# Kernel tuning notes

Measured on AMD Instinct MI355X. Metric: run time of the kernel, lower is better.

## Reference

```python
import jax, jax.numpy as jnp
import numpy as np

N = 100000   # nodes
E = 500000   # edges
D = 128      # node_hidden_size
ED = 128     # edge_emb_dim
L = 8        # n_message_passes
H = 4        # num_heads
V = 8192     # node_vocab_size
G = 64       # num_graphs
A = 100      # num_actions
NFLOW = 8
NPOS = 64


def setup_inputs() -> dict:
    key = jax.random.key(0)
    ks = jax.random.split(key, 24)
    rn = lambda k, shape, s: jax.random.normal(k, shape, jnp.float32) * s
    inp = {}
    # graph tensors
    inp['x'] = jax.random.randint(ks[0], (N,), 0, V)
    inp['node_type'] = jax.random.randint(ks[1], (N,), 0, 2)
    inp['batch'] = jnp.sort(jax.random.randint(ks[2], (N,), 0, G))
    inp['edge_index'] = jax.random.randint(ks[3], (2, E), 0, N)
    inp['flow'] = jax.random.randint(ks[4], (E,), 0, NFLOW)
    inp['position'] = jax.random.randint(ks[5], (E,), 0, NPOS)
    inp['block'] = jax.random.randint(ks[6], (N,), 0, 4096)
    inp['num_graphs'] = G
    # parameters
    sd = 1.0 / np.sqrt(D)
    se = 1.0 / np.sqrt(ED)
    inp['emb_table'] = rn(ks[7], (V, D), 1.0)
    inp['flow_emb'] = rn(ks[8], (NFLOW, ED), 1.0)
    inp['pos_emb'] = rn(ks[9], (NPOS, ED), 1.0)
    inp['blk_emb'] = rn(ks[10], (2, ED), 1.0)
    inp['Wq'] = rn(ks[11], (L, D, D), sd)
    inp['Wk'] = rn(ks[12], (L, D, D), sd)
    inp['Wv'] = rn(ks[13], (L, D, D), sd)
    inp['Wek'] = rn(ks[14], (L, ED, D), se)
    inp['Wev'] = rn(ks[15], (L, ED, D), se)
    inp['Wo'] = rn(ks[16], (L, D, D), sd)
    inp['Weu'] = rn(ks[17], (L, 2 * D + ED, ED), 1.0 / np.sqrt(2 * D + ED))
    inp['QW1'] = rn(ks[18], (D + ED, D), 1.0 / np.sqrt(D + ED))
    inp['Qb1'] = jnp.zeros((D,), jnp.float32)
    inp['QW2'] = rn(ks[19], (D, A), sd)
    inp['Qb2'] = jnp.zeros((A,), jnp.float32)
    return inp


def _forward(x, node_type, batch, edge_index, flow, position, block, num_graphs,
             emb_table, flow_emb, pos_emb, blk_emb,
             Wq, Wk, Wv, Wek, Wev, Wo, Weu, QW1, Qb1, QW2, Qb2):
    src, dst = edge_index[0], edge_index[1]
    feat = emb_table[x]                                        # [N, D]
    # EdgeEncoding: flow-type + position embeddings + block-crossing indicator
    crossing = (block[src] != block[dst]).astype(jnp.int32)
    e = flow_emb[flow] + pos_emb[position] + blk_emb[crossing]  # [E, ED]

    Nn, Dd = feat.shape
    dh = Dd // H
    scale = 1.0 / np.sqrt(dh)
    n_layers = Wq.shape[0]
    for l in range(n_layers):
        q = (feat @ Wq[l]).reshape(Nn, H, dh)
        k = (feat @ Wk[l]).reshape(Nn, H, dh)
        v = (feat @ Wv[l]).reshape(Nn, H, dh)
        ek = (e @ Wek[l]).reshape(-1, H, dh)
        ev = (e @ Wev[l]).reshape(-1, H, dh)
        # per-edge attention logits, softmax over edges sharing a dst node
        scores = jnp.sum(q[dst] * (k[src] + ek), axis=-1) * scale  # [E, H]
        m = jax.lax.stop_gradient(
            jax.ops.segment_max(scores, dst, num_segments=Nn))
        ex = jnp.exp(scores - m[dst])
        den = jax.ops.segment_sum(ex, dst, num_segments=Nn)
        alpha = ex / (den[dst] + 1e-16)                            # [E, H]
        msg = alpha[..., None] * (v[src] + ev)                     # [E, H, dh]
        agg = jax.ops.segment_sum(msg, dst, num_segments=Nn).reshape(Nn, Dd)
        feat_new = jax.nn.relu(feat + agg @ Wo[l])
        e = jax.nn.relu(e + jnp.concatenate([feat[src], feat[dst], e], axis=-1) @ Weu[l])
        feat = feat_new

    # scatter_mean over instruction nodes (type == 0) per graph
    maskf = (node_type == 0).astype(feat.dtype)
    ncnt = jax.ops.segment_sum(maskf, batch, num_segments=num_graphs)
    gagg = jax.ops.segment_sum(feat * maskf[:, None], batch, num_segments=num_graphs)
    gagg = gagg / jnp.maximum(ncnt, 1.0)[:, None]
    # scatter_mean of edge features per graph (edge's graph = graph of its src node)
    eb = batch[src]
    ecnt = jax.ops.segment_sum(jnp.ones((e.shape[0],), e.dtype), eb, num_segments=num_graphs)
    eagg = jax.ops.segment_sum(e, eb, num_segments=num_graphs)
    eagg = eagg / jnp.maximum(ecnt, 1.0)[:, None]

    ga = jnp.concatenate([gagg, eagg], axis=-1)                    # [G, D+ED]
    h = jax.nn.relu(ga @ QW1 + Qb1)
    logits = h @ QW2 + Qb2
    return jax.nn.log_softmax(logits, axis=-1)


def reference(x, node_type, batch, edge_index, flow, position, block, num_graphs,
              emb_table, flow_emb, pos_emb, blk_emb,
              Wq, Wk, Wv, Wek, Wev, Wo, Weu, QW1, Qb1, QW2, Qb2):
    return _forward(x, node_type, batch, edge_index, flow, position, block,
                    int(num_graphs), emb_table, flow_emb, pos_emb, blk_emb,
                    Wq, Wk, Wv, Wek, Wev, Wo, Weu, QW1, Qb1, QW2, Qb2)
```

## Files before the change

kernel.cpp:

```cpp
#include <hip/hip_runtime.h>
#include <stdint.h>

#define NN 100000
#define NE 500000
#define DD 128
#define NL 8
#define NG 64
#define NA 100
#define DET_PAIRS 65536

typedef unsigned short u16;
typedef unsigned int u32;
typedef __attribute__((ext_vector_type(8))) short short8;
typedef __attribute__((ext_vector_type(4))) float f32x4;

union U4 { uint4 v; u16 s[8]; };

__device__ __forceinline__ float b2f(u16 u){ union{u32 i; float f;} x; x.i=((u32)u)<<16; return x.f; }
__device__ __forceinline__ u16 f2b(float f){ union{float f; u32 i;} x; x.f=f; u32 b=x.i; b += 0x7fffu + ((b>>16)&1u); return (u16)(b>>16); }

__global__ void zero_k(int* __restrict__ p, int n){
  int i = blockIdx.x*256 + threadIdx.x;
  if (i < n) p[i] = 0;
}
__global__ void diag_k(u16* __restrict__ out, int n, float val){
  int i = blockIdx.x*256 + threadIdx.x;
  if (i < n) out[i] = f2b(val);
}

__global__ void detect_k(const u16* __restrict__ raw, int* __restrict__ flags){
  int i = blockIdx.x*256 + threadIdx.x;
  int ok = 0;
  if (i < DET_PAIRS){
    u16 v = raw[2*i];
    int e = (v>>7)&0xFF;
    ok = ((e >= 107 && e <= 147) || ((v & 0x7FFFu) == 0)) ? 1 : 0;
  }
  unsigned long long b = __ballot(ok);
  if ((threadIdx.x & 63) == 0) atomicAdd(&flags[2], (int)__popcll(b));
}
__global__ void flagset_k(int* __restrict__ flags){
  if (threadIdx.x==0) flags[0] = (flags[2] < DET_PAIRS/2) ? 1 : 0;
}
__global__ void tobf16_k(const void* __restrict__ in, u16* __restrict__ out, int n,
                         const int* __restrict__ flags){
  int i = blockIdx.x*256 + threadIdx.x;
  if (i >= n) return;
  if (flags[0]) out[i] = f2b(((const float*)in)[i]);
  else          out[i] = ((const u16*)in)[i];
}
__global__ void convT_k(const void* __restrict__ in, u16* __restrict__ out, int L, int K, int Nn,
                        const int* __restrict__ flags){
  int id = blockIdx.x*256 + threadIdx.x;
  int tot = L*K*Nn;
  if (id >= tot) return;
  int l = id/(K*Nn); int r = id - l*K*Nn;
  int k = r/Nn; int n = r - k*Nn;
  u16 v;
  if (flags[0]) v = f2b(((const float*)in)[id]);
  else          v = ((const u16*)in)[id];
  out[(size_t)l*K*Nn + (size_t)n*K + k] = v;
}

__global__ void featinit_k(const int* __restrict__ x, const u16* __restrict__ emb, u16* __restrict__ feat){
  int id = blockIdx.x*256 + threadIdx.x;
  if (id >= NN*16) return;
  int row = id>>4, c8 = (id&15)*8;
  int g = x[row];
  *(uint4*)(feat + (size_t)row*DD + c8) = *(const uint4*)(emb + (size_t)g*DD + c8);
}

__global__ void count_k(const int* __restrict__ dst, int* __restrict__ cnt){
  int e = blockIdx.x*256 + threadIdx.x;
  if (e < NE) atomicAdd(&cnt[dst[e]], 1);
}
__global__ void scan1_k(const int* __restrict__ cnt, int* __restrict__ excl, int* __restrict__ bsum, int n){
  __shared__ int sh[256];
  int t = threadIdx.x, g = blockIdx.x*256 + t;
  int v = (g<n) ? cnt[g] : 0;
  sh[t] = v; __syncthreads();
  for (int d=1; d<256; d<<=1){
    int xv = (t>=d) ? sh[t-d] : 0;
    __syncthreads();
    sh[t] += xv;
    __syncthreads();
  }
  if (g<n) excl[g] = sh[t]-v;
  if (t==255) bsum[blockIdx.x] = sh[255];
}
__global__ void scan2_k(int* __restrict__ bsum, int nb){
  if (threadIdx.x==0 && blockIdx.x==0){
    int a=0;
    for (int i=0;i<nb;i++){ int x=bsum[i]; bsum[i]=a; a+=x; }
  }
}
__global__ void scan3_k(const int* __restrict__ excl, const int* __restrict__ bsum,
                        int* __restrict__ offs, int* __restrict__ cursor, int n, int total){
  int g = blockIdx.x*256 + threadIdx.x;
  if (g < n){ int o = excl[g] + bsum[g>>8]; offs[g]=o; cursor[g]=o; }
  if (g==0) offs[n] = total;
}
__global__ void fill_k(const int* __restrict__ dst, int* __restrict__ cursor, int* __restrict__ perm){
  int e = blockIdx.x*256 + threadIdx.x;
  if (e < NE){ int p = atomicAdd(&cursor[dst[e]], 1); perm[p] = e; }
}
__global__ void make_sorted_k(const int* __restrict__ perm, const int* __restrict__ src,
                              const int* __restrict__ dst, int* __restrict__ srcs, int* __restrict__ dsts){
  int i = blockIdx.x*256 + threadIdx.x;
  if (i < NE){ int ed = perm[i]; srcs[i] = src[ed]; dsts[i] = dst[ed]; }
}

__global__ void edgeinit_k(const int* __restrict__ perm, const int* __restrict__ flow,
                           const int* __restrict__ pos, const int* __restrict__ blk,
                           const int* __restrict__ srcs, const int* __restrict__ dsts,
                           const int* __restrict__ batch,
                           const u16* __restrict__ flow_emb, const u16* __restrict__ pos_emb,
                           const u16* __restrict__ blk_emb,
                           u16* __restrict__ e, int* __restrict__ ebgs){
  int id = blockIdx.x*256 + threadIdx.x;
  if (id >= NE*16) return;
  int i = id>>4, c8 = (id&15)*8;
  int ed = perm[i];
  int s = srcs[i], d = dsts[i];
  int cross = (blk[s] != blk[d]) ? 1 : 0;
  U4 a,b,c,o;
  a.v = *(const uint4*)(flow_emb + (size_t)flow[ed]*DD + c8);
  b.v = *(const uint4*)(pos_emb  + (size_t)pos[ed]*DD + c8);
  c.v = *(const uint4*)(blk_emb  + (size_t)cross*DD + c8);
  #pragma unroll
  for (int j=0;j<8;j++) o.s[j] = f2b(b2f(a.s[j]) + b2f(b.s[j]) + b2f(c.s[j]));
  *(uint4*)(e + (size_t)i*DD + c8) = o.v;
  if ((id&15)==0) ebgs[i] = batch[s];
}

__global__ __launch_bounds__(256,4) void gemm_k(
    const u16* A0, const int* __restrict__ i0,
    const u16* A1, const int* __restrict__ i1,
    const u16* A2, const int* __restrict__ i2, int nchunks,
    const u16* __restrict__ Bt, int Ktot,
    const u16* res, int do_relu, int res_lds,
    u16* C, int M)
{
  __shared__ u16 As[128*128];
  int t = threadIdx.x;
  int mbase = blockIdx.x*128;
  int lane = t & 63, w = t>>6;
  int wrow = (w>>1)*64, wcol = (w&1)*64;
  int rl_w = t>>4, gw = t&15;
  int l15 = lane & 15, quad = lane>>4;
  f32x4 acc[4][4];
  #pragma unroll
  for (int mi=0;mi<4;mi++)
    #pragma unroll
    for (int ni=0;ni<4;ni++){ acc[mi][ni][0]=0.f; acc[mi][ni][1]=0.f; acc[mi][ni][2]=0.f; acc[mi][ni][3]=0.f; }

  for (int c=0; c<nchunks; c++){
    const u16* A = (c==0)?A0:((c==1)?A1:A2);
    const int* idx = (c==0)?i0:((c==1)?i1:i2);
    if (c > 0) __syncthreads();
    #pragma unroll
    for (int i=0;i<8;i++){
      int gm = mbase + rl_w + 16*i;
      uint4 av = make_uint4(0u,0u,0u,0u);
      if (gm < M){
        size_t grow = idx ? (size_t)idx[gm] : (size_t)gm;
        av = *(const uint4*)(A + grow*DD + gw*8);
      }
      *(uint4*)(As + (size_t)(i*256 + rl_w*16 + (gw ^ rl_w))*8) = av;
    }
    __syncthreads();
    #pragma unroll
    for (int kk=0;kk<4;kk++){
      int kg = kk*4 + quad;
      short8 af[4], bfr[4];
      #pragma unroll
      for (int mi=0;mi<4;mi++)
        af[mi] = *(const short8*)(As + (size_t)(((wrow>>4)+mi)*256 + l15*16 + (kg ^ l15))*8);
      #pragma unroll
      for (int ni=0;ni<4;ni++)
        bfr[ni] = *(const short8*)(Bt + (size_t)(wcol + ni*16 + l15)*Ktot + c*128 + kg*8);
      #pragma unroll
      for (int mi=0;mi<4;mi++)
        #pragma unroll
        for (int ni=0;ni<4;ni++)
          acc[mi][ni] = __builtin_amdgcn_mfma_f32_16x16x32_bf16(af[mi], bfr[ni], acc[mi][ni], 0, 0, 0);
    }
  }

  if (res_lds){
    #pragma unroll
    for (int mi=0;mi<4;mi++){
      #pragma unroll
      for (int r4=0;r4<4;r4++){
        int row = wrow + mi*16 + quad*4 + r4;
        #pragma unroll
        for (int ni=0;ni<4;ni++){
          int col = wcol + ni*16 + l15;
          float r = b2f(As[(row>>4)*2048 + (row&15)*128 + (((col>>3) ^ (row&15))<<3) + (col&7)]);
          float vv = acc[mi][ni][r4] + r;
          if (do_relu && vv < 0.f) vv = 0.f;
          acc[mi][ni][r4] = vv;
        }
      }
    }
  }
  __syncthreads();
  #pragma unroll
  for (int mi=0;mi<4;mi++){
    #pragma unroll
    for (int r4=0;r4<4;r4++){
      int row = wrow + mi*16 + quad*4 + r4;
      #pragma unroll
      for (int ni=0;ni<4;ni++){
        int col = wcol + ni*16 + l15;
        As[row*128 + ((((col>>3) ^ (row&15))<<3)) + (col&7)] = f2b(acc[mi][ni][r4]);
      }
    }
  }
  __syncthreads();
  #pragma unroll
  for (int i=0;i<8;i++){
    int row = rl_w + 16*i;
    int gm = mbase + row;
    if (gm >= M) continue;
    U4 av; av.v = *(const uint4*)(As + row*128 + ((gw ^ (row&15))<<3));
    if (res_lds){
      *(uint4*)(C + (size_t)gm*DD + gw*8) = av.v;
      continue;
    }
    float vals[8];
    #pragma unroll
    for (int j=0;j<8;j++) vals[j] = b2f(av.s[j]);
    if (res){
      U4 rv; rv.v = *(const uint4*)(res + (size_t)gm*DD + gw*8);
      #pragma unroll
      for (int j=0;j<8;j++) vals[j] += b2f(rv.s[j]);
    }
    U4 ov;
    #pragma unroll
    for (int j=0;j<8;j++){
      float v = vals[j];
      if (do_relu && v < 0.f) v = 0.f;
      ov.s[j] = f2b(v);
    }
    *(uint4*)(C + (size_t)gm*DD + gw*8) = ov.v;
  }
}

__global__ __launch_bounds__(256,4) void scores_fused_k(
    const u16* __restrict__ E, const u16* __restrict__ WekT,
    const u16* __restrict__ q, const u16* __restrict__ k,
    const int* __restrict__ srcs, const int* __restrict__ dsts,
    float* __restrict__ sc)
{
  __shared__ u16 As[128*128];
  int t = threadIdx.x;
  int ebase = blockIdx.x*128;
  int lane = t & 63, w = t>>6;
  int wrow = (w>>1)*64, wcol = (w&1)*64;
  int rl_w = t>>4, gw = t&15;
  int l15 = lane & 15, quad = lane>>4;
  #pragma unroll
  for (int i=0;i<8;i++){
    int gm = ebase + rl_w + 16*i;
    uint4 av = make_uint4(0u,0u,0u,0u);
    if (gm < NE) av = *(const uint4*)(E + (size_t)gm*DD + gw*8);
    *(uint4*)(As + (size_t)(i*256 + rl_w*16 + (gw ^ rl_w))*8) = av;
  }
  __syncthreads();
  f32x4 acc[4][4];
  #pragma unroll
  for (int mi=0;mi<4;mi++)
    #pragma unroll
    for (int ni=0;ni<4;ni++){ acc[mi][ni][0]=0.f; acc[mi][ni][1]=0.f; acc[mi][ni][2]=0.f; acc[mi][ni][3]=0.f; }
  #pragma unroll
  for (int kk=0;kk<4;kk++){
    int kg = kk*4 + quad;
    short8 af[4], bfr[4];
    #pragma unroll
    for (int mi=0;mi<4;mi++)
      af[mi] = *(const short8*)(As + (size_t)(((wrow>>4)+mi)*256 + l15*16 + (kg ^ l15))*8);
    #pragma unroll
    for (int ni=0;ni<4;ni++)
      bfr[ni] = *(const short8*)(WekT + (size_t)(wcol + ni*16 + l15)*DD + kg*8);
    #pragma unroll
    for (int mi=0;mi<4;mi++)
      #pragma unroll
      for (int ni=0;ni<4;ni++)
        acc[mi][ni] = __builtin_amdgcn_mfma_f32_16x16x32_bf16(af[mi], bfr[ni], acc[mi][ni], 0, 0, 0);
  }
  __syncthreads();
  #pragma unroll
  for (int mi=0;mi<4;mi++){
    #pragma unroll
    for (int r4=0;r4<4;r4++){
      int row = wrow + mi*16 + quad*4 + r4;
      #pragma unroll
      for (int ni=0;ni<4;ni++){
        int col = wcol + ni*16 + l15;
        As[row*128 + ((((col>>3) ^ (row&15))<<3)) + (col&7)] = f2b(acc[mi][ni][r4]);
      }
    }
  }
  __syncthreads();
  const float scale = 0.17677669529663689f;
  for (int pid = t; pid < 512; pid += 256){
    int le = pid>>2, h = pid&3;
    int e = ebase + le;
    if (e >= NE) continue;
    int s = srcs[e], d = dsts[e];
    float dot = 0.f;
    #pragma unroll
    for (int j4=0;j4<4;j4++){
      int off = h*32 + j4*8;
      U4 qv, kv, ev;
      qv.v = *(const uint4*)(q + (size_t)d*DD + off);
      kv.v = *(const uint4*)(k + (size_t)s*DD + off);
      ev.v = *(const uint4*)(As + le*128 + ((((h*4+j4) ^ (le&15))<<3)));
      #pragma unroll
      for (int j=0;j<8;j++) dot += b2f(qv.s[j]) * (b2f(kv.s[j]) + b2f(ev.s[j]));
    }
    sc[(size_t)e*4 + h] = dot * scale;
  }
}

__global__ __launch_bounds__(256,4) void nodeagg_k(
    const float* __restrict__ sc, const u16* __restrict__ v,
    const u16* __restrict__ E, const int* __restrict__ srcs,
    const int* __restrict__ offs, const u16* __restrict__ WevL,
    u16* __restrict__ agg)
{
  __shared__ float sh[16*4*129];
  int t = threadIdx.x;
  int n16 = t>>4;
  int node = blockIdx.x*16 + n16;
  int sub = t & 15;
  int hown = sub>>2;
  int offc = sub*8;
  int beg = 0, end = 0;
  if (node < NN){ beg = offs[node]; end = offs[node+1]; }
  float m[4] = {-1e30f,-1e30f,-1e30f,-1e30f};
  float den[4] = {0.f,0.f,0.f,0.f};
  for (int i=beg;i<end;i++){
    float4 s4 = *(const float4*)(sc + (size_t)i*4);
    float ss[4] = {s4.x, s4.y, s4.z, s4.w};
    #pragma unroll
    for (int h=0;h<4;h++){
      float mn = fmaxf(m[h], ss[h]);
      den[h] = den[h]*__expf(m[h]-mn) + __expf(ss[h]-mn);
      m[h] = mn;
    }
  }
  float inv[4];
  #pragma unroll
  for (int h=0;h<4;h++) inv[h] = 1.0f/(den[h] + 1e-16f);
  float uh[4][8];
  #pragma unroll
  for (int h=0;h<4;h++)
    #pragma unroll
    for (int j=0;j<8;j++) uh[h][j]=0.f;
  float accv[8] = {0.f,0.f,0.f,0.f,0.f,0.f,0.f,0.f};
  for (int i=beg;i<end;i++){
    float4 s4 = *(const float4*)(sc + (size_t)i*4);
    float al[4] = { __expf(s4.x-m[0])*inv[0], __expf(s4.y-m[1])*inv[1],
                    __expf(s4.z-m[2])*inv[2], __expf(s4.w-m[3])*inv[3] };
    U4 ee; ee.v = *(const uint4*)(E + (size_t)i*DD + offc);
    #pragma unroll
    for (int j=0;j<8;j++){
      float ev = b2f(ee.s[j]);
      #pragma unroll
      for (int h=0;h<4;h++) uh[h][j] += al[h]*ev;
    }
    U4 vv; vv.v = *(const uint4*)(v + (size_t)srcs[i]*DD + offc);
    #pragma unroll
    for (int j=0;j<8;j++) accv[j] += al[hown]*b2f(vv.s[j]);
  }
  #pragma unroll
  for (int h=0;h<4;h++)
    #pragma unroll
    for (int j=0;j<8;j++) sh[(n16*4 + h)*129 + offc + j] = uh[h][j];
  __syncthreads();
  if (node >= NN) return;
  float o8[8];
  #pragma unroll
  for (int j=0;j<8;j++) o8[j] = accv[j];
  int base = (n16*4 + hown)*129;
  for (int kk=0;kk<128;kk+=4){
    float u0 = sh[base+kk], u1 = sh[base+kk+1], u2 = sh[base+kk+2], u3 = sh[base+kk+3];
    U4 w0,w1,w2,w3;
    w0.v = *(const uint4*)(WevL + (size_t)kk*DD + offc);
    w1.v = *(const uint4*)(WevL + (size_t)(kk+1)*DD + offc);
    w2.v = *(const uint4*)(WevL + (size_t)(kk+2)*DD + offc);
    w3.v = *(const uint4*)(WevL + (size_t)(kk+3)*DD + offc);
    #pragma unroll
    for (int j=0;j<8;j++)
      o8[j] += u0*b2f(w0.s[j]) + u1*b2f(w1.s[j]) + u2*b2f(w2.s[j]) + u3*b2f(w3.s[j]);
  }
  U4 o;
  #pragma unroll
  for (int j=0;j<8;j++) o.s[j] = f2b(o8[j]);
  *(uint4*)(agg + (size_t)node*DD + offc) = o.v;
}

__global__ void hist_k(const int* __restrict__ gid, const int* __restrict__ mask, int n,
                       int* __restrict__ hist){
  __shared__ int lh[NG];
  int t = threadIdx.x;
  if (t < NG) lh[t]=0;
  __syncthreads();
  int i = blockIdx.x*256 + t;
  if (i < n && (!mask || mask[i]==0)) atomicAdd(&lh[gid[i]], 1);
  __syncthreads();
  if (t < NG && lh[t]) atomicAdd(&hist[t], lh[t]);
}
__global__ void scan64_k(const int* __restrict__ hist, int* __restrict__ base, int* __restrict__ cur){
  if (threadIdx.x==0){
    int a=0;
    for (int g=0; g<NG; g++){ base[g]=a; cur[g]=a; a+=hist[g]; }
    base[NG]=a;
  }
}
__global__ void fillperm_k(const int* __restrict__ gid, const int* __restrict__ mask, int n,
                           int* __restrict__ cur, int* __restrict__ operm){
  __shared__ int lh[NG];
  __shared__ int lb[NG];
  int t = threadIdx.x;
  if (t < NG) lh[t]=0;
  __syncthreads();
  int i = blockIdx.x*256 + t;
  int g=-1, r=0;
  if (i < n && (!mask || mask[i]==0)){ g = gid[i]; r = atomicAdd(&lh[g], 1); }
  __syncthreads();
  if (t < NG && lh[t]) lb[t] = atomicAdd(&cur[t], lh[t]);
  __syncthreads();
  if (g >= 0) operm[lb[g] + r] = i;
}
__global__ __launch_bounds__(256,4) void poolsum_k(
    const u16* __restrict__ feat, const int* __restrict__ operm,
    const int* __restrict__ base, int chunks, float* __restrict__ outsum)
{
  __shared__ float sh[16*128];
  int g = blockIdx.x / chunks, c = blockIdx.x % chunks;
  int beg = base[g], end = base[g+1];
  int len = end - beg;
  int cb = beg + (int)(((long long)len*c)/chunks);
  int ce = beg + (int)(((long long)len*(c+1))/chunks);
  int t = threadIdx.x, grp = t>>4, sub = t&15;
  float acc[8] = {0.f,0.f,0.f,0.f,0.f,0.f,0.f,0.f};
  for (int i = cb+grp; i < ce; i += 16){
    int r = operm[i];
    U4 fv; fv.v = *(const uint4*)(feat + (size_t)r*DD + sub*8);
    #pragma unroll
    for (int j=0;j<8;j++) acc[j] += b2f(fv.s[j]);
  }
  #pragma unroll
  for (int j=0;j<8;j++) sh[grp*128 + sub*8 + j] = acc[j];
  __syncthreads();
  if (t < 128){
    float s = 0.f;
    #pragma unroll
    for (int r=0;r<16;r++) s += sh[r*128 + t];
    if (s != 0.f) atomicAdd(&outsum[g*DD + t], s);
  }
}

__global__ void ganorm_k(const float* __restrict__ gsum, const int* __restrict__ ncnt,
                         const float* __restrict__ esum, const int* __restrict__ ecnt,
                         float* __restrict__ ga){
  int id = blockIdx.x*256 + threadIdx.x;
  if (id >= NG*256) return;
  int g = id>>8, c = id&255;
  float v;
  if (c < 128) v = gsum[g*DD + c] / fmaxf((float)ncnt[g], 1.f);
  else         v = esum[g*DD + (c-128)] / fmaxf((float)ecnt[g], 1.f);
  ga[(size_t)g*256 + c] = v;
}

__global__ void mlp1_k(const float* __restrict__ ga, const u16* __restrict__ QW1,
                       const u16* __restrict__ Qb1, float* __restrict__ h){
  int o = blockIdx.x*256 + threadIdx.x;
  if (o >= NG*DD) return;
  int g = o>>7, j = o&127;
  float s = b2f(Qb1[j]);
  #pragma unroll 4
  for (int kq=0;kq<256;kq++) s += ga[(size_t)g*256 + kq] * b2f(QW1[(size_t)kq*DD + j]);
  h[o] = fmaxf(s, 0.f);
}

__global__ __launch_bounds__(128) void mlp2_k(const float* __restrict__ h, const u16* __restrict__ QW2,
                       const u16* __restrict__ Qb2, void* __restrict__ out, const int* __restrict__ flags){
  __shared__ float lsh[NA];
  __shared__ float red[128];
  int g = blockIdx.x, t = threadIdx.x;
  float s = -1e30f;
  if (t < NA){
    float acc = b2f(Qb2[t]);
    #pragma unroll 4
    for (int kq=0;kq<DD;kq++) acc += h[(size_t)g*DD + kq] * b2f(QW2[(size_t)kq*NA + t]);
    lsh[t] = acc; s = acc;
  }
  red[t] = s; __syncthreads();
  for (int d=64; d>0; d>>=1){ if (t<d) red[t] = fmaxf(red[t], red[t+d]); __syncthreads(); }
  float m = red[0]; __syncthreads();
  float ex = (t < NA) ? __expf(lsh[t]-m) : 0.f;
  red[t] = ex; __syncthreads();
  for (int d=64; d>0; d>>=1){ if (t<d) red[t] += red[t+d]; __syncthreads(); }
  float lse = m + __logf(red[0]);
  if (t < NA){
    float r = lsh[t]-lse;
    if (flags[0]) ((float*)out)[(size_t)g*NA + t] = r;
    else          ((u16*)out)[(size_t)g*NA + t]  = f2b(r);
  }
}

extern "C" void kernel_launch(void* const* d_in, const int* in_sizes, int n_in,
                              void* d_out, int out_size, void* d_ws, size_t ws_size,
                              hipStream_t stream) {
  (void)in_sizes; (void)n_in;
  const int* x      = (const int*)d_in[0];
  const int* ntype  = (const int*)d_in[1];
  const int* batch  = (const int*)d_in[2];
  const int* eidx   = (const int*)d_in[3];
  const int* src    = eidx;
  const int* dstp   = eidx + NE;
  const int* flow   = (const int*)d_in[4];
  const int* pos    = (const int*)d_in[5];
  const int* blk    = (const int*)d_in[6];

  char* p = (char*)d_ws;
  auto alloc = [&](size_t bytes)->char* {
    char* r = p; p += (bytes + 255) & ~(size_t)255; return r;
  };
  u16* embB  = (u16*)alloc((size_t)8192*DD*2);
  u16* flowB = (u16*)alloc(8*DD*2);
  u16* posB  = (u16*)alloc(64*DD*2);
  u16* blkB  = (u16*)alloc(2*DD*2);
  const size_t WSZb = (size_t)NL*DD*DD*2;
  u16* WevB = (u16*)alloc(WSZb);
  u16* QW1B = (u16*)alloc((size_t)256*DD*2);
  u16* Qb1B = (u16*)alloc(DD*2);
  u16* QW2B = (u16*)alloc((size_t)DD*NA*2);
  u16* Qb2B = (u16*)alloc(NA*2);
  u16* WqT  = (u16*)alloc(WSZb);
  u16* WkT  = (u16*)alloc(WSZb);
  u16* WvT  = (u16*)alloc(WSZb);
  u16* WekT = (u16*)alloc(WSZb);
  u16* WoT  = (u16*)alloc(WSZb);
  u16* WeuT = (u16*)alloc((size_t)NL*DD*384*2);
  const size_t NB = (size_t)NN*DD*2;
  u16* A  = (u16*)alloc(NB);
  u16* QB = (u16*)alloc(NB);
  u16* KB = (u16*)alloc(NB);
  u16* SCRATCH = (u16*)alloc(NB);
  const size_t EB = (size_t)NE*DD*2;
  u16* E = (u16*)alloc(EB);
  float* scores = (float*)alloc((size_t)NE*4*4);
  int* srcs   = (int*)alloc((size_t)NE*4);
  int* dsts   = (int*)alloc((size_t)NE*4);
  int* ebgs   = (int*)alloc((size_t)NE*4);
  int* offs   = (int*)alloc((size_t)(NN+1)*4);
  float* gsum = (float*)alloc((size_t)NG*DD*4);
  float* esum = (float*)alloc((size_t)NG*DD*4);
  float* ga = (float*)alloc((size_t)NG*256*4);
  float* h  = (float*)alloc((size_t)NG*DD*4);
  int* flags = (int*)alloc(16);

  char* q = (char*)SCRATCH;
  auto suballoc = [&](size_t bytes)->char* {
    char* r = q; q += (bytes + 255) & ~(size_t)255; return r;
  };
  int* perm   = (int*)suballoc((size_t)NE*4);
  int* cnt    = (int*)suballoc((size_t)NN*4);
  int* excl   = (int*)suballoc((size_t)NN*4);
  int* bsum   = (int*)suballoc(1024*4);
  int* cursor = (int*)suballoc((size_t)NN*4);
  int* eperm  = (int*)suballoc((size_t)NE*4);
  int* nperm  = (int*)suballoc((size_t)NN*4);
  int* ehist  = (int*)suballoc(NG*4);
  int* ebase  = (int*)suballoc((NG+1)*4);
  int* ecur   = (int*)suballoc(NG*4);
  int* nhist  = (int*)suballoc(NG*4);
  int* nbase  = (int*)suballoc((NG+1)*4);
  int* ncur   = (int*)suballoc(NG*4);

  size_t needed = (size_t)(p - (char*)d_ws);
  if (needed > ws_size){
    diag_k<<<(out_size+255)/256,256,0,stream>>>((u16*)d_out, out_size, (float)(ws_size>>20));
    return;
  }

  zero_k<<<1,256,0,stream>>>(flags, 4);
  detect_k<<<(DET_PAIRS+255)/256,256,0,stream>>>((const u16*)d_in[8], flags);
  flagset_k<<<1,64,0,stream>>>(flags);
  auto conv = [&](int idx, u16* dst, int n){
    tobf16_k<<<(n+255)/256,256,0,stream>>>(d_in[idx], dst, n, flags);
  };
  auto convT = [&](int idx, u16* dst, int L, int K, int Nc){
    int n = L*K*Nc;
    convT_k<<<(n+255)/256,256,0,stream>>>(d_in[idx], dst, L, K, Nc, flags);
  };
  conv(8,  embB,  8192*DD);
  conv(9,  flowB, 8*DD);
  conv(10, posB,  64*DD);
  conv(11, blkB,  2*DD);
  convT(12, WqT,  NL, DD, DD);
  convT(13, WkT,  NL, DD, DD);
  convT(14, WvT,  NL, DD, DD);
  convT(15, WekT, NL, DD, DD);
  conv(16, WevB, NL*DD*DD);
  convT(17, WoT,  NL, DD, DD);
  convT(18, WeuT, NL, 384, DD);
  conv(19, QW1B, 256*DD);
  conv(20, Qb1B, DD);
  conv(21, QW2B, DD*NA);
  conv(22, Qb2B, NA);

  zero_k<<<(NN+255)/256,256,0,stream>>>(cnt, NN);
  count_k<<<(NE+255)/256,256,0,stream>>>(dstp, cnt);
  int nb = (NN+255)/256;
  scan1_k<<<nb,256,0,stream>>>(cnt, excl, bsum, NN);
  scan2_k<<<1,64,0,stream>>>(bsum, nb);
  scan3_k<<<nb,256,0,stream>>>(excl, bsum, offs, cursor, NN, NE);
  fill_k<<<(NE+255)/256,256,0,stream>>>(dstp, cursor, perm);
  make_sorted_k<<<(NE+255)/256,256,0,stream>>>(perm, src, dstp, srcs, dsts);
  featinit_k<<<(NN*16+255)/256,256,0,stream>>>(x, embB, A);
  edgeinit_k<<<(NE*16+255)/256,256,0,stream>>>(perm, flow, pos, blk, srcs, dsts, batch,
                                               flowB, posB, blkB, E, ebgs);

  dim3 gN((NN+127)/128), gE((NE+127)/128);
  for (int l=0; l<NL; l++){
    const u16* wq  = WqT  + (size_t)l*DD*DD;
    const u16* wk  = WkT  + (size_t)l*DD*DD;
    const u16* wv  = WvT  + (size_t)l*DD*DD;
    const u16* wek = WekT + (size_t)l*DD*DD;
    const u16* wo  = WoT  + (size_t)l*DD*DD;
    const u16* wevL= WevB + (size_t)l*DD*DD;
    const u16* weu = WeuT + (size_t)l*DD*384;

    gemm_k<<<gN,256,0,stream>>>(A,nullptr,nullptr,nullptr,nullptr,nullptr,1, wq,128, nullptr,0,0, QB, NN);
    gemm_k<<<gN,256,0,stream>>>(A,nullptr,nullptr,nullptr,nullptr,nullptr,1, wk,128, nullptr,0,0, KB, NN);
    scores_fused_k<<<gE,256,0,stream>>>(E, wek, QB, KB, srcs, dsts, scores);
    gemm_k<<<gN,256,0,stream>>>(A,nullptr,nullptr,nullptr,nullptr,nullptr,1, wv,128, nullptr,0,0, KB, NN);
    nodeagg_k<<<(NN+15)/16,256,0,stream>>>(scores, KB, E, srcs, offs, wevL, QB);
    gemm_k<<<gE,256,0,stream>>>(A,srcs, A,dsts, E,nullptr, 3, weu,384, nullptr,1,1, E, NE);
    gemm_k<<<gN,256,0,stream>>>(QB,nullptr,nullptr,nullptr,nullptr,nullptr,1, wo,128, A,1,0, A, NN);
  }

  zero_k<<<1,256,0,stream>>>(ehist, NG);
  zero_k<<<1,256,0,stream>>>(nhist, NG);
  zero_k<<<(NG*DD+255)/256,256,0,stream>>>((int*)gsum, NG*DD);
  zero_k<<<(NG*DD+255)/256,256,0,stream>>>((int*)esum, NG*DD);
  hist_k<<<(NE+255)/256,256,0,stream>>>(ebgs, nullptr, NE, ehist);
  hist_k<<<(NN+255)/256,256,0,stream>>>(batch, ntype, NN, nhist);
  scan64_k<<<1,64,0,stream>>>(ehist, ebase, ecur);
  scan64_k<<<1,64,0,stream>>>(nhist, nbase, ncur);
  fillperm_k<<<(NE+255)/256,256,0,stream>>>(ebgs, nullptr, NE, ecur, eperm);
  fillperm_k<<<(NN+255)/256,256,0,stream>>>(batch, ntype, NN, ncur, nperm);
  const int ECH = 16, NCH = 4;
  poolsum_k<<<NG*ECH,256,0,stream>>>(E, eperm, ebase, ECH, esum);
  poolsum_k<<<NG*NCH,256,0,stream>>>(A, nperm, nbase, NCH, gsum);
  ganorm_k<<<(NG*256+255)/256,256,0,stream>>>(gsum, nhist, esum, ehist, ga);
  mlp1_k<<<(NG*DD+255)/256,256,0,stream>>>(ga, QW1B, Qb1B, h);
  mlp2_k<<<NG,128,0,stream>>>(h, QW2B, Qb2B, d_out, flags);
}
```

Baseline: 4.566 ms.

## Batch QKV projections into one launch and co-schedule edge-update with Wo GEMM

The GEMM body becomes a device function shared by two new kernels. One computes the Q, K and V projections in a single launch, picking the weight matrix from grid.y, so V is written to its own buffer. The other runs the edge-update GEMM and the output-projection GEMM in one launch by splitting the block range. To avoid a read/write hazard on node features, the Wo result is ping-ponged into the former K buffer. This cuts per-layer launches from seven to four and lets the two independent GEMMs overlap instead of draining the GPU between them, at the cost of aliasing scratch memory and extra buffer juggling.

```diff
diff --git a/kernel.cpp b/kernel.cpp
--- a/kernel.cpp
+++ b/kernel.cpp
@@ -133,17 +133,16 @@
   if ((id&15)==0) ebgs[i] = batch[s];
 }
 
-__global__ __launch_bounds__(256,4) void gemm_k(
-    const u16* A0, const int* __restrict__ i0,
-    const u16* A1, const int* __restrict__ i1,
-    const u16* A2, const int* __restrict__ i2, int nchunks,
-    const u16* __restrict__ Bt, int Ktot,
+__device__ __forceinline__ void gemm_body(
+    u16* As, int t, int bx,
+    const u16* A0, const int* i0,
+    const u16* A1, const int* i1,
+    const u16* A2, const int* i2, int nchunks,
+    const u16* Bt, int Ktot,
     const u16* res, int do_relu, int res_lds,
     u16* C, int M)
 {
-  __shared__ u16 As[128*128];
-  int t = threadIdx.x;
-  int mbase = blockIdx.x*128;
+  int mbase = bx*128;
   int lane = t & 63, w = t>>6;
   int wrow = (w>>1)*64, wcol = (w&1)*64;
   int rl_w = t>>4, gw = t&15;
@@ -244,6 +243,35 @@
       ov.s[j] = f2b(v);
     }
     *(uint4*)(C + (size_t)gm*DD + gw*8) = ov.v;
+  }
+}
+
+__global__ __launch_bounds__(256,4) void qkv3_k(
+    const u16* __restrict__ A, const u16* __restrict__ B0,
+    const u16* __restrict__ B1, const u16* __restrict__ B2,
+    u16* __restrict__ C0, u16* __restrict__ C1, u16* __restrict__ C2, int M)
+{
+  __shared__ u16 As[128*128];
+  const u16* B = (blockIdx.y==0)?B0:((blockIdx.y==1)?B1:B2);
+  u16* C = (blockIdx.y==0)?C0:((blockIdx.y==1)?C1:C2);
+  gemm_body(As, threadIdx.x, blockIdx.x,
+            A,nullptr,nullptr,nullptr,nullptr,nullptr,1, B,128, nullptr,0,0, C, M);
+}
+
+__global__ __launch_bounds__(256,4) void ew_k(
+    const u16* eA0, const int* ei0, const u16* eA1, const int* ei1,
+    const u16* eA2, const int* ei2,
+    const u16* __restrict__ eBt, u16* eC, int split,
+    const u16* wA, const u16* __restrict__ wBt, const u16* wres, u16* wC)
+{
+  __shared__ u16 As[128*128];
+  int bx = blockIdx.x;
+  if (bx < split){
+    gemm_body(As, threadIdx.x, bx,
+              eA0,ei0, eA1,ei1, eA2,ei2, 3, eBt,384, nullptr,1,1, eC, NE);
+  } else {
+    gemm_body(As, threadIdx.x, bx - split,
+              wA,nullptr,nullptr,nullptr,nullptr,nullptr,1, wBt,128, wres,1,0, wC, NN);
   }
 }
 
@@ -565,6 +593,7 @@
   float* h  = (float*)alloc((size_t)NG*DD*4);
   int* flags = (int*)alloc(16);
 
+  u16* VB = SCRATCH;
   char* q = (char*)SCRATCH;
   auto suballoc = [&](size_t bytes)->char* {
     char* r = q; q += (bytes + 255) & ~(size_t)255; return r;
@@ -627,7 +656,8 @@
   edgeinit_k<<<(NE*16+255)/256,256,0,stream>>>(perm, flow, pos, blk, srcs, dsts, batch,
                                                flowB, posB, blkB, E, ebgs);
 
-  dim3 gN((NN+127)/128), gE((NE+127)/128);
+  int gNx = (NN+127)/128, gEx = (NE+127)/128;
+  u16 *F = A, *K2 = KB;
   for (int l=0; l<NL; l++){
     const u16* wq  = WqT  + (size_t)l*DD*DD;
     const u16* wk  = WkT  + (size_t)l*DD*DD;
@@ -637,13 +667,12 @@
     const u16* wevL= WevB + (size_t)l*DD*DD;
     const u16* weu = WeuT + (size_t)l*DD*384;
 
-    gemm_k<<<gN,256,0,stream>>>(A,nullptr,nullptr,nullptr,nullptr,nullptr,1, wq,128, nullptr,0,0, QB, NN);
-    gemm_k<<<gN,256,0,stream>>>(A,nullptr,nullptr,nullptr,nullptr,nullptr,1, wk,128, nullptr,0,0, KB, NN);
-    scores_fused_k<<<gE,256,0,stream>>>(E, wek, QB, KB, srcs, dsts, scores);
-    gemm_k<<<gN,256,0,stream>>>(A,nullptr,nullptr,nullptr,nullptr,nullptr,1, wv,128, nullptr,0,0, KB, NN);
-    nodeagg_k<<<(NN+15)/16,256,0,stream>>>(scores, KB, E, srcs, offs, wevL, QB);
-    gemm_k<<<gE,256,0,stream>>>(A,srcs, A,dsts, E,nullptr, 3, weu,384, nullptr,1,1, E, NE);
-    gemm_k<<<gN,256,0,stream>>>(QB,nullptr,nullptr,nullptr,nullptr,nullptr,1, wo,128, A,1,0, A, NN);
+    qkv3_k<<<dim3(gNx,3),256,0,stream>>>(F, wq, wk, wv, QB, K2, VB, NN);
+    scores_fused_k<<<gEx,256,0,stream>>>(E, wek, QB, K2, srcs, dsts, scores);
+    nodeagg_k<<<(NN+15)/16,256,0,stream>>>(scores, VB, E, srcs, offs, wevL, QB);
+    ew_k<<<gEx+gNx,256,0,stream>>>(F,srcs, F,dsts, E,nullptr, weu, E, gEx,
+                                   QB, wo, F, K2);
+    u16* tmp = F; F = K2; K2 = tmp;
   }
 
   zero_k<<<1,256,0,stream>>>(ehist, NG);
@@ -658,7 +687,7 @@
   fillperm_k<<<(NN+255)/256,256,0,stream>>>(batch, ntype, NN, ncur, nperm);
   const int ECH = 16, NCH = 4;
   poolsum_k<<<NG*ECH,256,0,stream>>>(E, eperm, ebase, ECH, esum);
-  poolsum_k<<<NG*NCH,256,0,stream>>>(A, nperm, nbase, NCH, gsum);
+  poolsum_k<<<NG*NCH,256,0,stream>>>(F, nperm, nbase, NCH, gsum);
   ganorm_k<<<(NG*256+255)/256,256,0,stream>>>(gsum, nhist, esum, ehist, ga);
   mlp1_k<<<(NG*DD+255)/256,256,0,stream>>>(ga, QW1B, Qb1B, h);
   mlp2_k<<<NG,128,0,stream>>>(h, QW2B, Qb2B, d_out, flags);
```

After: 4.616 ms. About the same (+1.1%).
